# Kernel optimization log

Hardware: AMD Instinct MI355X
Metric: run time of the kernel (lower is better)

## Reference

```python
import jax, jax.numpy as jnp
import numpy as np

H = 5  # LSTM hidden size


def _lstm_layer(x, Wih, Whh, bih, bhh):
    # x: [B, T, D]; Wih: [4H, D]; Whh: [4H, H]; biases: [4H]
    B, T, _ = x.shape
    # precompute input contribution with one big GEMM (torch gate order i,f,g,o)
    xg = jnp.einsum('btd,gd->btg', x, Wih) + bih + bhh  # [B,T,4H]
    xg = jnp.swapaxes(xg, 0, 1)  # [T,B,4H]
    WhhT = Whh.T

    def step(carry, g_t):
        h, c = carry
        g = g_t + h @ WhhT
        i, f, gg, o = jnp.split(g, 4, axis=-1)
        i = jax.nn.sigmoid(i)
        f = jax.nn.sigmoid(f)
        gg = jnp.tanh(gg)
        o = jax.nn.sigmoid(o)
        c = f * c + i * gg
        h = o * jnp.tanh(c)
        return (h, c), h

    h0 = jnp.zeros((B, H), x.dtype)
    c0 = jnp.zeros((B, H), x.dtype)
    _, hs = jax.lax.scan(step, (h0, c0), xg)
    return jnp.swapaxes(hs, 0, 1)  # [B,T,H]


def _stacked_lstm(x, params):
    for (Wih, Whh, bih, bhh) in params:
        x = _lstm_layer(x, Wih, Whh, bih, bhh)
    return x


def setup_inputs() -> dict:
    key = jax.random.key(0)
    ks = jax.random.split(key, 24)
    B, T, D = 512, 1024, 225
    s = 1.0 / np.sqrt(H)

    def u(k, shape):
        return jax.random.uniform(k, shape, jnp.float32, -s, s)

    inp = {"x": jax.random.normal(ks[0], (B, T, D), jnp.float32)}
    # lstm1: layer0 input D=225, layer1 input H=5
    inp["l1_Wih0"] = u(ks[1], (4 * H, D)); inp["l1_Whh0"] = u(ks[2], (4 * H, H))
    inp["l1_bih0"] = u(ks[3], (4 * H,)); inp["l1_bhh0"] = u(ks[4], (4 * H,))
    inp["l1_Wih1"] = u(ks[5], (4 * H, H)); inp["l1_Whh1"] = u(ks[6], (4 * H, H))
    inp["l1_bih1"] = u(ks[7], (4 * H,)); inp["l1_bhh1"] = u(ks[8], (4 * H,))
    inp["fc1_W"] = u(ks[9], (H, H)); inp["fc1_b"] = u(ks[10], (H,))
    # lstm2: both layers input H=5
    inp["l2_Wih0"] = u(ks[11], (4 * H, H)); inp["l2_Whh0"] = u(ks[12], (4 * H, H))
    inp["l2_bih0"] = u(ks[13], (4 * H,)); inp["l2_bhh0"] = u(ks[14], (4 * H,))
    inp["l2_Wih1"] = u(ks[15], (4 * H, H)); inp["l2_Whh1"] = u(ks[16], (4 * H, H))
    inp["l2_bih1"] = u(ks[17], (4 * H,)); inp["l2_bhh1"] = u(ks[18], (4 * H,))
    inp["fc2_W"] = u(ks[19], (H, H)); inp["fc2_b"] = u(ks[20], (H,))
    return inp


def reference(x, l1_Wih0, l1_Whh0, l1_bih0, l1_bhh0,
              l1_Wih1, l1_Whh1, l1_bih1, l1_bhh1,
              fc1_W, fc1_b,
              l2_Wih0, l2_Whh0, l2_bih0, l2_bhh0,
              l2_Wih1, l2_Whh1, l2_bih1, l2_bhh1,
              fc2_W, fc2_b):
    # dropout layers are identity in inference mode
    h = _stacked_lstm(x, [(l1_Wih0, l1_Whh0, l1_bih0, l1_bhh0),
                          (l1_Wih1, l1_Whh1, l1_bih1, l1_bhh1)])
    h = jax.nn.relu(h @ fc1_W.T + fc1_b)
    h = _stacked_lstm(h, [(l2_Wih0, l2_Whh0, l2_bih0, l2_bhh0),
                          (l2_Wih1, l2_Whh1, l2_bih1, l2_bhh1)])
    return jax.nn.sigmoid(h @ fc2_W.T + fc2_b)
```

## Files before the change

kernel.cpp:

```cpp
#include <hip/hip_runtime.h>
#include <math.h>

#define T_STEPS 1024
#define B_SIZE  512
#define D_IN    225
#define WT_K    228
#define LOG2E   1.4426950408889634f

typedef float f32x2 __attribute__((ext_vector_type(2)));

__device__ __forceinline__ float fexp2(float x) {
#if __has_builtin(__builtin_amdgcn_exp2f)
  return __builtin_amdgcn_exp2f(x);
#else
  return exp2f(x);
#endif
}
__device__ __forceinline__ float frcp(float x) {
#if __has_builtin(__builtin_amdgcn_rcpf)
  return __builtin_amdgcn_rcpf(x);
#else
  return 1.0f / x;
#endif
}
#define SIG(x) frcp(1.0f + fexp2((x) * (-LOG2E)))
#define TH(x)  fmaf(2.0f, frcp(1.0f + fexp2((x) * (-2.0f * LOG2E))), -1.0f)

#define GL16(gp, lp) __builtin_amdgcn_global_load_lds(                          \
    (const __attribute__((address_space(1))) void*)(gp),                        \
    (__attribute__((address_space(3))) void*)(lp), 16, 0, 0)
#define GL4(gp, lp)  __builtin_amdgcn_global_load_lds(                          \
    (const __attribute__((address_space(1))) void*)(gp),                        \
    (__attribute__((address_space(3))) void*)(lp), 4, 0, 0)

#define WAIT_VM0() do {                                                         \
    asm volatile("s_waitcnt vmcnt(0)" ::: "memory");                            \
    __builtin_amdgcn_sched_barrier(0);                                          \
  } while (0)
#define WAIT_VM10() do {                                                        \
    asm volatile("s_waitcnt vmcnt(10)" ::: "memory");                           \
    __builtin_amdgcn_sched_barrier(0);                                          \
  } while (0)

__global__ __launch_bounds__(256)
void prep_wt(const float* __restrict__ Wih, const float* __restrict__ bih,
             const float* __restrict__ bhh, float* __restrict__ wt2)
{
  int i = blockIdx.x * 256 + threadIdx.x;
  int g = i / WT_K, kk = i - g * WT_K;
  float v = 0.f;
  if (g < 20 && kk < 225) v = Wih[g * 225 + kk];
  if (i >= 4560 && i < 4580) v = bih[i - 4560] + bhh[i - 4560];
  wt2[i] = v;
}

__global__ __launch_bounds__(256)
void xg_gemm(const float* __restrict__ x, const float* __restrict__ wtg,
             float* __restrict__ xg)
{
  __shared__ __align__(16) float xs[64 * D_IN];
  __shared__ __align__(16) float wt[4608];
  const int tid  = threadIdx.x;
  const int lane = tid & 63;
  const int w    = __builtin_amdgcn_readfirstlane(tid >> 6);

  {
    int n0 = (w < 2) ? 5 : 4;
    int c0 = (w < 2) ? w * 5 : 10 + (w - 2) * 4;
    for (int m = 0; m < n0; ++m)
      GL16(wtg + (c0 + m) * 256 + lane * 4, wt + (c0 + m) * 256);
  }
  {
    const float* src = x + (size_t)blockIdx.x * (64 * D_IN);
    for (int m = 0; m < 14; ++m)
      GL16(src + (w * 14 + m) * 256 + lane * 4, xs + (w * 14 + m) * 256);
    if (w == 0) GL4(src + 14336 + lane, xs + 14336);
  }
  __syncthreads();

  const float* wr = wt + (5 * w) * WT_K;
  float acc[5];
#pragma unroll
  for (int j = 0; j < 5; ++j) acc[j] = wt[4560 + 5 * w + j];
  const float* xr = xs + lane * D_IN;

#pragma unroll 8
  for (int kb = 0; kb < 224; kb += 4) {
    float x0 = xr[kb], x1 = xr[kb + 1], x2 = xr[kb + 2], x3 = xr[kb + 3];
#pragma unroll
    for (int j = 0; j < 5; ++j) {
      const float4 wv = *(const float4*)(wr + j * WT_K + kb);
      acc[j] = fmaf(x0, wv.x, acc[j]);
      acc[j] = fmaf(x1, wv.y, acc[j]);
      acc[j] = fmaf(x2, wv.z, acc[j]);
      acc[j] = fmaf(x3, wv.w, acc[j]);
    }
  }
  {
    float xl = xr[224];
#pragma unroll
    for (int j = 0; j < 5; ++j) acc[j] = fmaf(xl, wr[j * WT_K + 224], acc[j]);
  }
  float* op = xg + ((size_t)blockIdx.x * 64 + lane) * 20 + w;
#pragma unroll
  for (int j = 0; j < 5; ++j) op[4 * j] = acc[j];
}

__global__ __launch_bounds__(64)
void lstm_fused(const float* __restrict__ xg, float* __restrict__ out,
              const float* __restrict__ l1_Whh0,
              const float* __restrict__ l1_Wih1, const float* __restrict__ l1_Whh1,
              const float* __restrict__ l1_bih1, const float* __restrict__ l1_bhh1,
              const float* __restrict__ fc1_W,  const float* __restrict__ fc1_b,
              const float* __restrict__ l2_Wih0, const float* __restrict__ l2_Whh0,
              const float* __restrict__ l2_bih0, const float* __restrict__ l2_bhh0,
              const float* __restrict__ l2_Wih1, const float* __restrict__ l2_Whh1,
              const float* __restrict__ l2_bih1, const float* __restrict__ l2_bhh1,
              const float* __restrict__ fc2_W,  const float* __restrict__ fc2_b)
{
  __shared__ __align__(16) float xq[2][2][1280];
  __shared__ float outb[2][64][5];
  const int lane  = threadIdx.x & 63;
  const int half  = lane >> 5;
  const int l32   = lane & 31;
  const int stage = (l32 < 30) ? (l32 / 5) : 6;
  const int u     = (l32 < 30) ? (l32 - stage * 5) : 0;
  const int b0    = blockIdx.x * 2;

  const bool is_l0   = (stage == 0);
  const bool is_relu = (stage == 2);
  const bool is_fc   = (stage == 2) || (stage == 5);
  const bool is_fc2  = (stage == 5);

  float wi[4][5] = {}, wh[4][5] = {}, bs[4] = {};
  if (stage == 0) {
#pragma unroll
    for (int q = 0; q < 4; ++q)
#pragma unroll
      for (int j = 0; j < 5; ++j) wh[q][j] = l1_Whh0[(u + 5 * q) * 5 + j];
  } else if (stage == 1) {
#pragma unroll
    for (int q = 0; q < 4; ++q) {
#pragma unroll
      for (int j = 0; j < 5; ++j) {
        wi[q][j] = l1_Wih1[(u + 5 * q) * 5 + j];
        wh[q][j] = l1_Whh1[(u + 5 * q) * 5 + j];
      }
      bs[q] = l1_bih1[u + 5 * q] + l1_bhh1[u + 5 * q];
    }
  } else if (stage == 3) {
#pragma unroll
    for (int q = 0; q < 4; ++q) {
#pragma unroll
      for (int j = 0; j < 5; ++j) {
        wi[q][j] = l2_Wih0[(u + 5 * q) * 5 + j];
        wh[q][j] = l2_Whh0[(u + 5 * q) * 5 + j];
      }
      bs[q] = l2_bih0[u + 5 * q] + l2_bhh0[u + 5 * q];
    }
  } else if (stage == 4) {
#pragma unroll
    for (int q = 0; q < 4; ++q) {
#pragma unroll
      for (int j = 0; j < 5; ++j) {
        wi[q][j] = l2_Wih1[(u + 5 * q) * 5 + j];
        wh[q][j] = l2_Whh1[(u + 5 * q) * 5 + j];
      }
      bs[q] = l2_bih1[u + 5 * q] + l2_bhh1[u + 5 * q];
    }
  } else if (stage == 2) {
#pragma unroll
    for (int j = 0; j < 5; ++j) wi[0][j] = fc1_W[u * 5 + j];
    bs[0] = fc1_b[u];
  } else if (stage == 5) {
#pragma unroll
    for (int j = 0; j < 5; ++j) wi[0][j] = fc2_W[u * 5 + j];
    bs[0] = fc2_b[u];
  }

  f32x2 wi01[5], wi23[5], wh01[5], wh23[5];
#pragma unroll
  for (int j = 0; j < 5; ++j) {
    wi01[j] = f32x2{wi[0][j], wi[1][j]};
    wi23[j] = f32x2{wi[2][j], wi[3][j]};
    wh01[j] = f32x2{wh[0][j], wh[1][j]};
    wh23[j] = f32x2{wh[2][j], wh[3][j]};
  }
  const f32x2 bs01 = f32x2{bs[0], bs[1]};
  const f32x2 bs23 = f32x2{bs[2], bs[3]};

  int ii[5], ih[5];
  const int bse = half * 32;
  const int inb = (stage >= 1 && stage <= 5) ? (stage - 1) * 5 : 0;
  const int hb_ = (stage <= 5) ? stage * 5 : 0;
#pragma unroll
  for (int j = 0; j < 5; ++j) {
    ii[j] = (bse + inb + j) * 4;
    ih[j] = (bse + hb_ + j) * 4;
  }

  const float* obf = &outb[0][0][0];
  float* outbase = out + (size_t)b0 * T_STEPS * 5;
  int lof[10], ofs[10];
  bool fg1[10], fg2[10];
#pragma unroll
  for (int i2 = 0; i2 < 10; ++i2) {
    int idx = i2 * 64 + lane;
    int e  = (idx >= 320) ? 1 : 0;
    int r  = idx - e * 320;
    int tq = r / 5;
    int j2 = r - tq * 5;
    lof[i2] = e * 320 + (((tq - 5) & 63) * 5) + j2;
    ofs[i2] = e * (T_STEPS * 5) + tq * 5 + j2;
    fg1[i2] = (tq >= 5);
    fg2[i2] = (tq < 5);
  }

  const float* src0 = xg + (size_t)(b0 + 0) * T_STEPS * 20;
  const float* src1 = xg + (size_t)(b0 + 1) * T_STEPS * 20;

#define STAGE_CHUNK(CH, BUF)                                                   \
  { const float* s0_ = src0 + (CH) * 1280;                                     \
    const float* s1_ = src1 + (CH) * 1280;                                     \
    float* d0_ = &xq[BUF][0][0];                                               \
    float* d1_ = &xq[BUF][1][0];                                               \
    _Pragma("unroll")                                                          \
    for (int m = 0; m < 5; ++m) {                                              \
      GL16(s0_ + m * 256 + lane * 4, d0_ + m * 256);                           \
      GL16(s1_ + m * 256 + lane * 4, d1_ + m * 256);                           \
    } }

#define TICK(QV, GUARDED, KVAL)                                                \
  { const int hvi_ = __float_as_int(hv);                                       \
    float inx[5], hhx[5];                                                      \
    _Pragma("unroll")                                                          \
    for (int j = 0; j < 5; ++j) {                                              \
      inx[j] = __int_as_float(__builtin_amdgcn_ds_bpermute(ii[j], hvi_));      \
      hhx[j] = __int_as_float(__builtin_amdgcn_ds_bpermute(ih[j], hvi_));      \
    }                                                                          \
    f32x2 a01 = is_l0 ? f32x2{(QV).x, (QV).y} : bs01;                          \
    f32x2 a23 = is_l0 ? f32x2{(QV).z, (QV).w} : bs23;                          \
    f32x2 b01, b23;                                                            \
    { const f32x2 h0 = f32x2{hhx[0], hhx[0]};                                  \
      b01 = wh01[0] * h0; b23 = wh23[0] * h0; }                                \
    _Pragma("unroll")                                                          \
    for (int j = 0; j < 5; ++j) {                                              \
      const f32x2 xj = f32x2{inx[j], inx[j]};                                  \
      a01 = __builtin_elementwise_fma(wi01[j], xj, a01);                       \
      a23 = __builtin_elementwise_fma(wi23[j], xj, a23);                       \
    }                                                                          \
    _Pragma("unroll")                                                          \
    for (int j = 1; j < 5; ++j) {                                              \
      const f32x2 hj = f32x2{hhx[j], hhx[j]};                                  \
      b01 = __builtin_elementwise_fma(wh01[j], hj, b01);                       \
      b23 = __builtin_elementwise_fma(wh23[j], hj, b23);                       \
    }                                                                          \
    const f32x2 pre01 = a01 + b01, pre23 = a23 + b23;                          \
    float i_ = SIG(pre01.x), f_ = SIG(pre01.y);                                \
    float g_ = TH(pre23.x),  o_ = SIG(pre23.y);                                \
    float cn = fmaf(f_, c, i_ * g_);                                           \
    float hl = o_ * TH(cn);                                                    \
    float fx = is_relu ? fmaxf(pre01.x, 0.0f) : i_;                            \
    float hn = is_fc ? fx : hl;                                                \
    if (GUARDED) { bool ok = (KVAL) >= stage; c = ok ? cn : c; hv = ok ? hn : hv; } \
    else         { c = cn; hv = hn; }                                          \
    if (is_fc2) outb[half][((KVAL) + 59) & 63][u] = i_;                        \
  }

#define LQ(T) (*(const float4*)(xqb + 20 * (T)))
#define MINQ(X) (((X) > 63) ? 63 : (X))

#define CHUNK_BODY(GUARDED)                                                    \
  { float4 qA = LQ(0), qB = LQ(1), qC = LQ(2), qD = LQ(3);                     \
    _Pragma("unroll")                                                          \
    for (int g4 = 0; g4 < 16; ++g4) {                                          \
      const int kk = g4 * 4;                                                   \
      TICK(qA, GUARDED, kk + 0)                                                \
      qA = LQ(MINQ(kk + 4));                                                   \
      TICK(qB, GUARDED, kk + 1)                                                \
      qB = LQ(MINQ(kk + 5));                                                   \
      TICK(qC, GUARDED, kk + 2)                                                \
      qC = LQ(MINQ(kk + 6));                                                   \
      TICK(qD, GUARDED, kk + 3)                                                \
      qD = LQ(MINQ(kk + 7));                                                   \
    } }

#define FLUSH(TBASE, MODE)                                                     \
  { _Pragma("unroll")                                                          \
    for (int i2 = 0; i2 < 10; ++i2) {                                          \
      float v = obf[lof[i2]];                                                  \
      bool ok = (MODE == 0) || ((MODE == 1) ? fg1[i2] : fg2[i2]);              \
      if (ok) outbase[ofs[i2] + (TBASE) * 5] = v;                              \
    } }

  float hv = 0.f, c = 0.f;

  STAGE_CHUNK(0, 0)
  WAIT_VM0();

  {
    STAGE_CHUNK(1, 1)
    const float* xqb = &xq[0][half][4 * u];
    CHUNK_BODY(true)
    FLUSH(-5, 1)
    WAIT_VM10();
  }
  for (int ch = 1; ch < 16; ++ch) {
    if (ch < 15) STAGE_CHUNK(ch + 1, (ch + 1) & 1)
    const float* xqb = &xq[ch & 1][half][4 * u];
    CHUNK_BODY(false)
    FLUSH(ch * 64 - 5, 0)
    WAIT_VM10();
  }
  {
    const float* xqb = &xq[0][half][4 * u];
    float4 qZ = LQ(0);
    TICK(qZ, false, 0)
    TICK(qZ, false, 1)
    TICK(qZ, false, 2)
    TICK(qZ, false, 3)
    TICK(qZ, false, 4)
    FLUSH(T_STEPS - 5, 2)
  }

#undef STAGE_CHUNK
#undef TICK
#undef LQ
#undef MINQ
#undef CHUNK_BODY
#undef FLUSH
}

extern "C" void kernel_launch(void* const* d_in, const int* in_sizes, int n_in,
                              void* d_out, int out_size, void* d_ws, size_t ws_size,
                              hipStream_t stream)
{
  const float* x        = (const float*)d_in[0];
  const float* l1_Wih0  = (const float*)d_in[1];
  const float* l1_Whh0  = (const float*)d_in[2];
  const float* l1_bih0  = (const float*)d_in[3];
  const float* l1_bhh0  = (const float*)d_in[4];
  const float* l1_Wih1  = (const float*)d_in[5];
  const float* l1_Whh1  = (const float*)d_in[6];
  const float* l1_bih1  = (const float*)d_in[7];
  const float* l1_bhh1  = (const float*)d_in[8];
  const float* fc1_W    = (const float*)d_in[9];
  const float* fc1_b    = (const float*)d_in[10];
  const float* l2_Wih0  = (const float*)d_in[11];
  const float* l2_Whh0  = (const float*)d_in[12];
  const float* l2_bih0  = (const float*)d_in[13];
  const float* l2_bhh0  = (const float*)d_in[14];
  const float* l2_Wih1  = (const float*)d_in[15];
  const float* l2_Whh1  = (const float*)d_in[16];
  const float* l2_bih1  = (const float*)d_in[17];
  const float* l2_bhh1  = (const float*)d_in[18];
  const float* fc2_W    = (const float*)d_in[19];
  const float* fc2_b    = (const float*)d_in[20];

  float* xg   = (float*)d_ws;
  float* wtws = xg + 10485760;
  float* out  = (float*)d_out;

  prep_wt<<<dim3(18), dim3(256), 0, stream>>>(l1_Wih0, l1_bih0, l1_bhh0, wtws);

  xg_gemm<<<dim3((B_SIZE * T_STEPS) / 64), dim3(256), 0, stream>>>(x, wtws, xg);

  lstm_fused<<<dim3(B_SIZE / 2), dim3(64), 0, stream>>>(
      xg, out, l1_Whh0, l1_Wih1, l1_Whh1, l1_bih1, l1_bhh1,
      fc1_W, fc1_b, l2_Wih0, l2_Whh0, l2_bih0, l2_bhh0,
      l2_Wih1, l2_Whh1, l2_bih1, l2_bhh1, fc2_W, fc2_b);
}
```

Baseline: 419.3 us.

## Restructure input GEMM to one wave per block and simplify LSTM tick loop

The input-projection GEMM now runs one 64-lane wave per block. That wave computes all 20 gates with packed FMA against a k-major transposed weight layout and writes each row as float4. This replaces four waves that each handled five gates, cutting block-level sync and making the output stores contiguous. The LSTM recurrent loop drops the four-deep register prefetch of xg rows in favour of a pointer-advancing tick with a plain LDS load, and the output ring index is simplified. The trade-offs are less parallelism per block in the GEMM, more LDS traffic per thread, and a possible loss of latency hiding in the serial recurrence.

```diff
diff --git a/kernel.cpp b/kernel.cpp
--- a/kernel.cpp
+++ b/kernel.cpp
@@ -4,7 +4,6 @@
 #define T_STEPS 1024
 #define B_SIZE  512
 #define D_IN    225
-#define WT_K    228
 #define LOG2E   1.4426950408889634f
 
 typedef float f32x2 __attribute__((ext_vector_type(2)));
@@ -47,63 +46,73 @@
              const float* __restrict__ bhh, float* __restrict__ wt2)
 {
   int i = blockIdx.x * 256 + threadIdx.x;
-  int g = i / WT_K, kk = i - g * WT_K;
   float v = 0.f;
-  if (g < 20 && kk < 225) v = Wih[g * 225 + kk];
-  if (i >= 4560 && i < 4580) v = bih[i - 4560] + bhh[i - 4560];
+  if (i < 4500) {
+    int k = i / 20, g = i - k * 20;
+    v = Wih[g * D_IN + k];
+  } else if (i < 4520) {
+    v = bih[i - 4500] + bhh[i - 4500];
+  }
   wt2[i] = v;
 }
 
-__global__ __launch_bounds__(256)
+__global__ __launch_bounds__(64)
 void xg_gemm(const float* __restrict__ x, const float* __restrict__ wtg,
              float* __restrict__ xg)
 {
   __shared__ __align__(16) float xs[64 * D_IN];
   __shared__ __align__(16) float wt[4608];
-  const int tid  = threadIdx.x;
-  const int lane = tid & 63;
-  const int w    = __builtin_amdgcn_readfirstlane(tid >> 6);
-
-  {
-    int n0 = (w < 2) ? 5 : 4;
-    int c0 = (w < 2) ? w * 5 : 10 + (w - 2) * 4;
-    for (int m = 0; m < n0; ++m)
-      GL16(wtg + (c0 + m) * 256 + lane * 4, wt + (c0 + m) * 256);
-  }
+  const int lane = threadIdx.x;
+
+#pragma unroll
+  for (int m = 0; m < 18; ++m)
+    GL16(wtg + m * 256 + lane * 4, wt + m * 256);
   {
     const float* src = x + (size_t)blockIdx.x * (64 * D_IN);
-    for (int m = 0; m < 14; ++m)
-      GL16(src + (w * 14 + m) * 256 + lane * 4, xs + (w * 14 + m) * 256);
-    if (w == 0) GL4(src + 14336 + lane, xs + 14336);
-  }
-  __syncthreads();
-
-  const float* wr = wt + (5 * w) * WT_K;
-  float acc[5];
-#pragma unroll
-  for (int j = 0; j < 5; ++j) acc[j] = wt[4560 + 5 * w + j];
+#pragma unroll
+    for (int m = 0; m < 56; ++m)
+      GL16(src + m * 256 + lane * 4, xs + m * 256);
+    GL4(src + 14336 + lane, xs + 14336);
+  }
+  WAIT_VM0();
+
+  f32x2 acc2[10];
+#pragma unroll
+  for (int p = 0; p < 10; ++p)
+    acc2[p] = f32x2{wt[4500 + 2 * p], wt[4500 + 2 * p + 1]};
   const float* xr = xs + lane * D_IN;
 
-#pragma unroll 8
-  for (int kb = 0; kb < 224; kb += 4) {
-    float x0 = xr[kb], x1 = xr[kb + 1], x2 = xr[kb + 2], x3 = xr[kb + 3];
-#pragma unroll
-    for (int j = 0; j < 5; ++j) {
-      const float4 wv = *(const float4*)(wr + j * WT_K + kb);
-      acc[j] = fmaf(x0, wv.x, acc[j]);
-      acc[j] = fmaf(x1, wv.y, acc[j]);
-      acc[j] = fmaf(x2, wv.z, acc[j]);
-      acc[j] = fmaf(x3, wv.w, acc[j]);
-    }
-  }
-  {
-    float xl = xr[224];
-#pragma unroll
-    for (int j = 0; j < 5; ++j) acc[j] = fmaf(xl, wr[j * WT_K + 224], acc[j]);
-  }
-  float* op = xg + ((size_t)blockIdx.x * 64 + lane) * 20 + w;
-#pragma unroll
-  for (int j = 0; j < 5; ++j) op[4 * j] = acc[j];
+#pragma unroll 5
+  for (int k = 0; k < D_IN; ++k) {
+    const float xv = xr[k];
+    const f32x2 xv2 = f32x2{xv, xv};
+    const float* wk = wt + k * 20;
+    const float4 wA = *(const float4*)(wk);
+    const float4 wB = *(const float4*)(wk + 4);
+    const float4 wC = *(const float4*)(wk + 8);
+    const float4 wD = *(const float4*)(wk + 12);
+    const float4 wE = *(const float4*)(wk + 16);
+    acc2[0] = __builtin_elementwise_fma(f32x2{wA.x, wA.y}, xv2, acc2[0]);
+    acc2[1] = __builtin_elementwise_fma(f32x2{wA.z, wA.w}, xv2, acc2[1]);
+    acc2[2] = __builtin_elementwise_fma(f32x2{wB.x, wB.y}, xv2, acc2[2]);
+    acc2[3] = __builtin_elementwise_fma(f32x2{wB.z, wB.w}, xv2, acc2[3]);
+    acc2[4] = __builtin_elementwise_fma(f32x2{wC.x, wC.y}, xv2, acc2[4]);
+    acc2[5] = __builtin_elementwise_fma(f32x2{wC.z, wC.w}, xv2, acc2[5]);
+    acc2[6] = __builtin_elementwise_fma(f32x2{wD.x, wD.y}, xv2, acc2[6]);
+    acc2[7] = __builtin_elementwise_fma(f32x2{wD.z, wD.w}, xv2, acc2[7]);
+    acc2[8] = __builtin_elementwise_fma(f32x2{wE.x, wE.y}, xv2, acc2[8]);
+    acc2[9] = __builtin_elementwise_fma(f32x2{wE.z, wE.w}, xv2, acc2[9]);
+  }
+
+#define AG(G) (((G) & 1) ? acc2[(G) >> 1].y : acc2[(G) >> 1].x)
+  float* op = xg + ((size_t)blockIdx.x * 64 + lane) * 20;
+#pragma unroll
+  for (int q = 0; q < 5; ++q) {
+    float4 o;
+    o.x = AG(q); o.y = AG(5 + q); o.z = AG(10 + q); o.w = AG(15 + q);
+    *(float4*)(op + 4 * q) = o;
+  }
+#undef AG
 }
 
 __global__ __launch_bounds__(64)
@@ -210,7 +219,7 @@
     int r  = idx - e * 320;
     int tq = r / 5;
     int j2 = r - tq * 5;
-    lof[i2] = e * 320 + (((tq - 5) & 63) * 5) + j2;
+    lof[i2] = e * 320 + tq * 5 + j2;
     ofs[i2] = e * (T_STEPS * 5) + tq * 5 + j2;
     fg1[i2] = (tq >= 5);
     fg2[i2] = (tq < 5);
@@ -230,16 +239,17 @@
       GL16(s1_ + m * 256 + lane * 4, d1_ + m * 256);                           \
     } }
 
-#define TICK(QV, GUARDED, KVAL)                                                \
-  { const int hvi_ = __float_as_int(hv);                                       \
+#define TICKR(GUARDED, KK)                                                     \
+  { const float4 Qv = *(const float4*)xqp;                                     \
+    const int hvi_ = __float_as_int(hv);                                       \
     float inx[5], hhx[5];                                                      \
     _Pragma("unroll")                                                          \
     for (int j = 0; j < 5; ++j) {                                              \
       inx[j] = __int_as_float(__builtin_amdgcn_ds_bpermute(ii[j], hvi_));      \
       hhx[j] = __int_as_float(__builtin_amdgcn_ds_bpermute(ih[j], hvi_));      \
     }                                                                          \
-    f32x2 a01 = is_l0 ? f32x2{(QV).x, (QV).y} : bs01;                          \
-    f32x2 a23 = is_l0 ? f32x2{(QV).z, (QV).w} : bs23;                          \
+    f32x2 a01 = is_l0 ? f32x2{Qv.x, Qv.y} : bs01;                              \
+    f32x2 a23 = is_l0 ? f32x2{Qv.z, Qv.w} : bs23;                              \
     f32x2 b01, b23;                                                            \
     { const f32x2 h0 = f32x2{hhx[0], hhx[0]};                                  \
       b01 = wh01[0] * h0; b23 = wh23[0] * h0; }                                \
@@ -262,28 +272,10 @@
     float hl = o_ * TH(cn);                                                    \
     float fx = is_relu ? fmaxf(pre01.x, 0.0f) : i_;                            \
     float hn = is_fc ? fx : hl;                                                \
-    if (GUARDED) { bool ok = (KVAL) >= stage; c = ok ? cn : c; hv = ok ? hn : hv; } \
+    if (GUARDED) { bool ok = (KK) >= stage; c = ok ? cn : c; hv = ok ? hn : hv; } \
     else         { c = cn; hv = hn; }                                          \
-    if (is_fc2) outb[half][((KVAL) + 59) & 63][u] = i_;                        \
-  }
-
-#define LQ(T) (*(const float4*)(xqb + 20 * (T)))
-#define MINQ(X) (((X) > 63) ? 63 : (X))
-
-#define CHUNK_BODY(GUARDED)                                                    \
-  { float4 qA = LQ(0), qB = LQ(1), qC = LQ(2), qD = LQ(3);                     \
-    _Pragma("unroll")                                                          \
-    for (int g4 = 0; g4 < 16; ++g4) {                                          \
-      const int kk = g4 * 4;                                                   \
-      TICK(qA, GUARDED, kk + 0)                                                \
-      qA = LQ(MINQ(kk + 4));                                                   \
-      TICK(qB, GUARDED, kk + 1)                                                \
-      qB = LQ(MINQ(kk + 5));                                                   \
-      TICK(qC, GUARDED, kk + 2)                                                \
-      qC = LQ(MINQ(kk + 6));                                                   \
-      TICK(qD, GUARDED, kk + 3)                                                \
-      qD = LQ(MINQ(kk + 7));                                                   \
-    } }
+    if (is_fc2) outb[half][KK][u] = i_;                                        \
+    xqp += 20; }
 
 #define FLUSH(TBASE, MODE)                                                     \
   { _Pragma("unroll")                                                          \
@@ -294,40 +286,31 @@
     } }
 
   float hv = 0.f, c = 0.f;
+  const float* xqp;
 
   STAGE_CHUNK(0, 0)
   WAIT_VM0();
 
-  {
-    STAGE_CHUNK(1, 1)
-    const float* xqb = &xq[0][half][4 * u];
-    CHUNK_BODY(true)
-    FLUSH(-5, 1)
-    WAIT_VM10();
-  }
+  STAGE_CHUNK(1, 1)
+  xqp = &xq[0][half][4 * u];
+  for (int kk = 0; kk < 64; ++kk) TICKR(true, kk)
+  FLUSH(-5, 1)
+  WAIT_VM10();
+
   for (int ch = 1; ch < 16; ++ch) {
     if (ch < 15) STAGE_CHUNK(ch + 1, (ch + 1) & 1)
-    const float* xqb = &xq[ch & 1][half][4 * u];
-    CHUNK_BODY(false)
+    xqp = &xq[ch & 1][half][4 * u];
+#pragma unroll 2
+    for (int kk = 0; kk < 64; ++kk) TICKR(false, kk)
     FLUSH(ch * 64 - 5, 0)
     WAIT_VM10();
   }
-  {
-    const float* xqb = &xq[0][half][4 * u];
-    float4 qZ = LQ(0);
-    TICK(qZ, false, 0)
-    TICK(qZ, false, 1)
-    TICK(qZ, false, 2)
-    TICK(qZ, false, 3)
-    TICK(qZ, false, 4)
-    FLUSH(T_STEPS - 5, 2)
-  }
+  xqp = &xq[0][half][4 * u];
+  for (int kk = 0; kk < 5; ++kk) TICKR(false, kk)
+  FLUSH(T_STEPS - 5, 2)
 
 #undef STAGE_CHUNK
-#undef TICK
-#undef LQ
-#undef MINQ
-#undef CHUNK_BODY
+#undef TICKR
 #undef FLUSH
 }
 
@@ -363,7 +346,7 @@
 
   prep_wt<<<dim3(18), dim3(256), 0, stream>>>(l1_Wih0, l1_bih0, l1_bhh0, wtws);
 
-  xg_gemm<<<dim3((B_SIZE * T_STEPS) / 64), dim3(256), 0, stream>>>(x, wtws, xg);
+  xg_gemm<<<dim3((B_SIZE * T_STEPS) / 64), dim3(64), 0, stream>>>(x, wtws, xg);
 
   lstm_fused<<<dim3(B_SIZE / 2), dim3(64), 0, stream>>>(
       xg, out, l1_Whh0, l1_Wih1, l1_Whh1, l1_bih1, l1_bhh1,
```

After: 452.5 us. +7.9%, slower.

## Decouple layer-input shuffles from recurrence by adding a one-tick lag per stage

Applied to the files above, without the earlier changes.

Each tick now uses the inter-stage input value fetched in the previous tick, so stage s runs two steps behind stage s-1 instead of one. The input-side FMAs and the shuffles for the next tick leave the recurrent critical path, and only the hidden-state permutes and gate math remain serial. The pipeline fill and drain grow from 5 to 10 steps, the output lag and flush offsets change to match, and the hand-unrolled prefetch of the xg queue is replaced by a pointer-increment load with unroll 2.

```diff
diff --git a/kernel.cpp b/kernel.cpp
--- a/kernel.cpp
+++ b/kernel.cpp
@@ -126,6 +126,7 @@
   const int stage = (l32 < 30) ? (l32 / 5) : 6;
   const int u     = (l32 < 30) ? (l32 - stage * 5) : 0;
   const int b0    = blockIdx.x * 2;
+  const int stg2  = stage * 2;
 
   const bool is_l0   = (stage == 0);
   const bool is_relu = (stage == 2);
@@ -210,10 +211,10 @@
     int r  = idx - e * 320;
     int tq = r / 5;
     int j2 = r - tq * 5;
-    lof[i2] = e * 320 + (((tq - 5) & 63) * 5) + j2;
+    lof[i2] = e * 320 + tq * 5 + j2;
     ofs[i2] = e * (T_STEPS * 5) + tq * 5 + j2;
-    fg1[i2] = (tq >= 5);
-    fg2[i2] = (tq < 5);
+    fg1[i2] = (tq >= 10);
+    fg2[i2] = (tq < 10);
   }
 
   const float* src0 = xg + (size_t)(b0 + 0) * T_STEPS * 20;
@@ -230,25 +231,27 @@
       GL16(s1_ + m * 256 + lane * 4, d1_ + m * 256);                           \
     } }
 
-#define TICK(QV, GUARDED, KVAL)                                                \
-  { const int hvi_ = __float_as_int(hv);                                       \
-    float inx[5], hhx[5];                                                      \
+#define TICK2(GUARDED, KK, INU, IND)                                           \
+  { const float4 Qv = *(const float4*)xqp;                                     \
+    const int hvi_ = __float_as_int(hv);                                       \
+    float hhx[5];                                                              \
+    _Pragma("unroll")                                                          \
+    for (int j = 0; j < 5; ++j)                                                \
+      hhx[j] = __int_as_float(__builtin_amdgcn_ds_bpermute(ih[j], hvi_));      \
+    f32x2 a01 = is_l0 ? f32x2{Qv.x, Qv.y} : bs01;                              \
+    f32x2 a23 = is_l0 ? f32x2{Qv.z, Qv.w} : bs23;                              \
     _Pragma("unroll")                                                          \
     for (int j = 0; j < 5; ++j) {                                              \
-      inx[j] = __int_as_float(__builtin_amdgcn_ds_bpermute(ii[j], hvi_));      \
-      hhx[j] = __int_as_float(__builtin_amdgcn_ds_bpermute(ih[j], hvi_));      \
+      const f32x2 xj = f32x2{INU[j], INU[j]};                                  \
+      a01 = __builtin_elementwise_fma(wi01[j], xj, a01);                       \
+      a23 = __builtin_elementwise_fma(wi23[j], xj, a23);                       \
     }                                                                          \
-    f32x2 a01 = is_l0 ? f32x2{(QV).x, (QV).y} : bs01;                          \
-    f32x2 a23 = is_l0 ? f32x2{(QV).z, (QV).w} : bs23;                          \
+    _Pragma("unroll")                                                          \
+    for (int j = 0; j < 5; ++j)                                                \
+      IND[j] = __int_as_float(__builtin_amdgcn_ds_bpermute(ii[j], hvi_));      \
     f32x2 b01, b23;                                                            \
     { const f32x2 h0 = f32x2{hhx[0], hhx[0]};                                  \
       b01 = wh01[0] * h0; b23 = wh23[0] * h0; }                                \
-    _Pragma("unroll")                                                          \
-    for (int j = 0; j < 5; ++j) {                                              \
-      const f32x2 xj = f32x2{inx[j], inx[j]};                                  \
-      a01 = __builtin_elementwise_fma(wi01[j], xj, a01);                       \
-      a23 = __builtin_elementwise_fma(wi23[j], xj, a23);                       \
-    }                                                                          \
     _Pragma("unroll")                                                          \
     for (int j = 1; j < 5; ++j) {                                              \
       const f32x2 hj = f32x2{hhx[j], hhx[j]};                                  \
@@ -262,28 +265,10 @@
     float hl = o_ * TH(cn);                                                    \
     float fx = is_relu ? fmaxf(pre01.x, 0.0f) : i_;                            \
     float hn = is_fc ? fx : hl;                                                \
-    if (GUARDED) { bool ok = (KVAL) >= stage; c = ok ? cn : c; hv = ok ? hn : hv; } \
+    if (GUARDED) { bool ok = (KK) >= stg2; c = ok ? cn : c; hv = ok ? hn : hv; } \
     else         { c = cn; hv = hn; }                                          \
-    if (is_fc2) outb[half][((KVAL) + 59) & 63][u] = i_;                        \
-  }
-
-#define LQ(T) (*(const float4*)(xqb + 20 * (T)))
-#define MINQ(X) (((X) > 63) ? 63 : (X))
-
-#define CHUNK_BODY(GUARDED)                                                    \
-  { float4 qA = LQ(0), qB = LQ(1), qC = LQ(2), qD = LQ(3);                     \
-    _Pragma("unroll")                                                          \
-    for (int g4 = 0; g4 < 16; ++g4) {                                          \
-      const int kk = g4 * 4;                                                   \
-      TICK(qA, GUARDED, kk + 0)                                                \
-      qA = LQ(MINQ(kk + 4));                                                   \
-      TICK(qB, GUARDED, kk + 1)                                                \
-      qB = LQ(MINQ(kk + 5));                                                   \
-      TICK(qC, GUARDED, kk + 2)                                                \
-      qC = LQ(MINQ(kk + 6));                                                   \
-      TICK(qD, GUARDED, kk + 3)                                                \
-      qD = LQ(MINQ(kk + 7));                                                   \
-    } }
+    if (is_fc2) outb[half][KK][u] = i_;                                        \
+    xqp += 20; }
 
 #define FLUSH(TBASE, MODE)                                                     \
   { _Pragma("unroll")                                                          \
@@ -294,40 +279,43 @@
     } }
 
   float hv = 0.f, c = 0.f;
+  float inxA[5] = {0, 0, 0, 0, 0};
+  float inxB[5] = {0, 0, 0, 0, 0};
+  const float* xqp;
 
   STAGE_CHUNK(0, 0)
   WAIT_VM0();
 
-  {
-    STAGE_CHUNK(1, 1)
-    const float* xqb = &xq[0][half][4 * u];
-    CHUNK_BODY(true)
-    FLUSH(-5, 1)
-    WAIT_VM10();
-  }
+  STAGE_CHUNK(1, 1)
+  xqp = &xq[0][half][4 * u];
+#pragma unroll 2
+  for (int kk = 0; kk < 64; kk += 2) {
+    TICK2(true, kk,     inxA, inxB)
+    TICK2(true, kk + 1, inxB, inxA)
+  }
+  FLUSH(-10, 1)
+  WAIT_VM10();
+
   for (int ch = 1; ch < 16; ++ch) {
     if (ch < 15) STAGE_CHUNK(ch + 1, (ch + 1) & 1)
-    const float* xqb = &xq[ch & 1][half][4 * u];
-    CHUNK_BODY(false)
-    FLUSH(ch * 64 - 5, 0)
+    xqp = &xq[ch & 1][half][4 * u];
+#pragma unroll 2
+    for (int kk = 0; kk < 64; kk += 2) {
+      TICK2(false, kk,     inxA, inxB)
+      TICK2(false, kk + 1, inxB, inxA)
+    }
+    FLUSH(ch * 64 - 10, 0)
     WAIT_VM10();
   }
-  {
-    const float* xqb = &xq[0][half][4 * u];
-    float4 qZ = LQ(0);
-    TICK(qZ, false, 0)
-    TICK(qZ, false, 1)
-    TICK(qZ, false, 2)
-    TICK(qZ, false, 3)
-    TICK(qZ, false, 4)
-    FLUSH(T_STEPS - 5, 2)
-  }
+  xqp = &xq[0][half][4 * u];
+  for (int kk = 0; kk < 10; kk += 2) {
+    TICK2(false, kk,     inxA, inxB)
+    TICK2(false, kk + 1, inxB, inxA)
+  }
+  FLUSH(T_STEPS - 10, 2)
 
 #undef STAGE_CHUNK
-#undef TICK
-#undef LQ
-#undef MINQ
-#undef CHUNK_BODY
+#undef TICK2
 #undef FLUSH
 }
 
```

New measurement: 435.2 us. 1.04x slower.

## Fuse input-projection GEMM into LSTM kernel with producer waves

Applied to the files above, without the earlier changes.

Removes the separate xg_gemm kernel and its 40MB intermediate xg buffer. The LSTM kernel now launches 256 threads per block: wave 0 runs the recurrent chain while waves 1 and 2 each load a 64-step slab of x for one batch element into LDS. Those producer waves compute the 20 gate pre-activations with packed FMAs against a k-major weight layout and double-buffer the results into xq for the next chunk. This trades an extra global round trip for per-chunk __syncthreads, much larger LDS use (about 140KB), and a producer that may stall the serial recurrence if its GEMM is slower than a chunk of ticks.

```diff
diff --git a/kernel.cpp b/kernel.cpp
--- a/kernel.cpp
+++ b/kernel.cpp
@@ -4,7 +4,6 @@
 #define T_STEPS 1024
 #define B_SIZE  512
 #define D_IN    225
-#define WT_K    228
 #define LOG2E   1.4426950408889634f
 
 typedef float f32x2 __attribute__((ext_vector_type(2)));
@@ -37,77 +36,25 @@
     asm volatile("s_waitcnt vmcnt(0)" ::: "memory");                            \
     __builtin_amdgcn_sched_barrier(0);                                          \
   } while (0)
-#define WAIT_VM10() do {                                                        \
-    asm volatile("s_waitcnt vmcnt(10)" ::: "memory");                           \
-    __builtin_amdgcn_sched_barrier(0);                                          \
-  } while (0)
 
 __global__ __launch_bounds__(256)
 void prep_wt(const float* __restrict__ Wih, const float* __restrict__ bih,
              const float* __restrict__ bhh, float* __restrict__ wt2)
 {
   int i = blockIdx.x * 256 + threadIdx.x;
-  int g = i / WT_K, kk = i - g * WT_K;
   float v = 0.f;
-  if (g < 20 && kk < 225) v = Wih[g * 225 + kk];
-  if (i >= 4560 && i < 4580) v = bih[i - 4560] + bhh[i - 4560];
+  if (i < 4500) {
+    int k = i / 20, g = i - k * 20;
+    v = Wih[g * D_IN + k];
+  } else if (i < 4520) {
+    v = bih[i - 4500] + bhh[i - 4500];
+  }
   wt2[i] = v;
 }
 
 __global__ __launch_bounds__(256)
-void xg_gemm(const float* __restrict__ x, const float* __restrict__ wtg,
-             float* __restrict__ xg)
-{
-  __shared__ __align__(16) float xs[64 * D_IN];
-  __shared__ __align__(16) float wt[4608];
-  const int tid  = threadIdx.x;
-  const int lane = tid & 63;
-  const int w    = __builtin_amdgcn_readfirstlane(tid >> 6);
-
-  {
-    int n0 = (w < 2) ? 5 : 4;
-    int c0 = (w < 2) ? w * 5 : 10 + (w - 2) * 4;
-    for (int m = 0; m < n0; ++m)
-      GL16(wtg + (c0 + m) * 256 + lane * 4, wt + (c0 + m) * 256);
-  }
-  {
-    const float* src = x + (size_t)blockIdx.x * (64 * D_IN);
-    for (int m = 0; m < 14; ++m)
-      GL16(src + (w * 14 + m) * 256 + lane * 4, xs + (w * 14 + m) * 256);
-    if (w == 0) GL4(src + 14336 + lane, xs + 14336);
-  }
-  __syncthreads();
-
-  const float* wr = wt + (5 * w) * WT_K;
-  float acc[5];
-#pragma unroll
-  for (int j = 0; j < 5; ++j) acc[j] = wt[4560 + 5 * w + j];
-  const float* xr = xs + lane * D_IN;
-
-#pragma unroll 8
-  for (int kb = 0; kb < 224; kb += 4) {
-    float x0 = xr[kb], x1 = xr[kb + 1], x2 = xr[kb + 2], x3 = xr[kb + 3];
-#pragma unroll
-    for (int j = 0; j < 5; ++j) {
-      const float4 wv = *(const float4*)(wr + j * WT_K + kb);
-      acc[j] = fmaf(x0, wv.x, acc[j]);
-      acc[j] = fmaf(x1, wv.y, acc[j]);
-      acc[j] = fmaf(x2, wv.z, acc[j]);
-      acc[j] = fmaf(x3, wv.w, acc[j]);
-    }
-  }
-  {
-    float xl = xr[224];
-#pragma unroll
-    for (int j = 0; j < 5; ++j) acc[j] = fmaf(xl, wr[j * WT_K + 224], acc[j]);
-  }
-  float* op = xg + ((size_t)blockIdx.x * 64 + lane) * 20 + w;
-#pragma unroll
-  for (int j = 0; j < 5; ++j) op[4 * j] = acc[j];
-}
-
-__global__ __launch_bounds__(64)
-void lstm_fused(const float* __restrict__ xg, float* __restrict__ out,
+void lstm_fused(const float* __restrict__ x, const float* __restrict__ wtg,
+              float* __restrict__ out,
               const float* __restrict__ l1_Whh0,
               const float* __restrict__ l1_Wih1, const float* __restrict__ l1_Whh1,
               const float* __restrict__ l1_bih1, const float* __restrict__ l1_bhh1,
@@ -119,8 +66,12 @@
               const float* __restrict__ fc2_W,  const float* __restrict__ fc2_b)
 {
   __shared__ __align__(16) float xq[2][2][1280];
+  __shared__ __align__(16) float xsl[2][14400];
+  __shared__ __align__(16) float wt[4608];
   __shared__ float outb[2][64][5];
-  const int lane  = threadIdx.x & 63;
+  const int tid   = threadIdx.x;
+  const int lane  = tid & 63;
+  const int wv    = tid >> 6;
   const int half  = lane >> 5;
   const int l32   = lane & 31;
   const int stage = (l32 < 30) ? (l32 / 5) : 6;
@@ -216,18 +167,49 @@
     fg2[i2] = (tq < 5);
   }
 
-  const float* src0 = xg + (size_t)(b0 + 0) * T_STEPS * 20;
-  const float* src1 = xg + (size_t)(b0 + 1) * T_STEPS * 20;
-
-#define STAGE_CHUNK(CH, BUF)                                                   \
-  { const float* s0_ = src0 + (CH) * 1280;                                     \
-    const float* s1_ = src1 + (CH) * 1280;                                     \
-    float* d0_ = &xq[BUF][0][0];                                               \
-    float* d1_ = &xq[BUF][1][0];                                               \
-    _Pragma("unroll")                                                          \
-    for (int m = 0; m < 5; ++m) {                                              \
-      GL16(s0_ + m * 256 + lane * 4, d0_ + m * 256);                           \
-      GL16(s1_ + m * 256 + lane * 4, d1_ + m * 256);                           \
+#define AG(G) (((G) & 1) ? acc2[(G) >> 1].y : acc2[(G) >> 1].x)
+#define PRODUCE(CH, BUF)                                                       \
+  { const int e_ = wv - 1;                                                     \
+    const float* slab_ = x + ((size_t)(b0 + e_) * T_STEPS + (CH) * 64) * 225;  \
+    float* dst_ = &xsl[e_][0];                                                 \
+    _Pragma("unroll")                                                          \
+    for (int m_ = 0; m_ < 56; ++m_)                                            \
+      GL16(slab_ + m_ * 256 + lane * 4, dst_ + m_ * 256);                      \
+    GL4(slab_ + 14336 + lane, dst_ + 14336);                                   \
+    WAIT_VM0();                                                                \
+    f32x2 acc2[10];                                                            \
+    _Pragma("unroll")                                                          \
+    for (int p_ = 0; p_ < 10; ++p_)                                            \
+      acc2[p_] = f32x2{wt[4500 + 2 * p_], wt[4500 + 2 * p_ + 1]};              \
+    const float* xr_ = dst_ + lane * 225;                                      \
+    _Pragma("unroll 3")                                                        \
+    for (int k_ = 0; k_ < 225; ++k_) {                                         \
+      const float xv_ = xr_[k_];                                               \
+      const f32x2 xv2_ = f32x2{xv_, xv_};                                      \
+      const float* wk_ = wt + k_ * 20;                                         \
+      const float4 wA_ = *(const float4*)(wk_);                                \
+      const float4 wB_ = *(const float4*)(wk_ + 4);                            \
+      const float4 wC_ = *(const float4*)(wk_ + 8);                            \
+      const float4 wD_ = *(const float4*)(wk_ + 12);                           \
+      const float4 wE_ = *(const float4*)(wk_ + 16);                           \
+      acc2[0] = __builtin_elementwise_fma(f32x2{wA_.x, wA_.y}, xv2_, acc2[0]); \
+      acc2[1] = __builtin_elementwise_fma(f32x2{wA_.z, wA_.w}, xv2_, acc2[1]); \
+      acc2[2] = __builtin_elementwise_fma(f32x2{wB_.x, wB_.y}, xv2_, acc2[2]); \
+      acc2[3] = __builtin_elementwise_fma(f32x2{wB_.z, wB_.w}, xv2_, acc2[3]); \
+      acc2[4] = __builtin_elementwise_fma(f32x2{wC_.x, wC_.y}, xv2_, acc2[4]); \
+      acc2[5] = __builtin_elementwise_fma(f32x2{wC_.z, wC_.w}, xv2_, acc2[5]); \
+      acc2[6] = __builtin_elementwise_fma(f32x2{wD_.x, wD_.y}, xv2_, acc2[6]); \
+      acc2[7] = __builtin_elementwise_fma(f32x2{wD_.z, wD_.w}, xv2_, acc2[7]); \
+      acc2[8] = __builtin_elementwise_fma(f32x2{wE_.x, wE_.y}, xv2_, acc2[8]); \
+      acc2[9] = __builtin_elementwise_fma(f32x2{wE_.z, wE_.w}, xv2_, acc2[9]); \
+    }                                                                          \
+    float* qp_ = &xq[BUF][e_][lane * 20];                                      \
+    _Pragma("unroll")                                                          \
+    for (int u_ = 0; u_ < 5; ++u_) {                                           \
+      float4 o_;                                                               \
+      o_.x = AG(u_);      o_.y = AG(5 + u_);                                   \
+      o_.z = AG(10 + u_); o_.w = AG(15 + u_);                                  \
+      *(float4*)(qp_ + 4 * u_) = o_;                                           \
     } }
 
 #define TICK(QV, GUARDED, KVAL)                                                \
@@ -295,24 +277,31 @@
 
   float hv = 0.f, c = 0.f;
 
-  STAGE_CHUNK(0, 0)
-  WAIT_VM0();
-
-  {
-    STAGE_CHUNK(1, 1)
-    const float* xqb = &xq[0][half][4 * u];
-    CHUNK_BODY(true)
-    FLUSH(-5, 1)
-    WAIT_VM10();
-  }
-  for (int ch = 1; ch < 16; ++ch) {
-    if (ch < 15) STAGE_CHUNK(ch + 1, (ch + 1) & 1)
-    const float* xqb = &xq[ch & 1][half][4 * u];
-    CHUNK_BODY(false)
-    FLUSH(ch * 64 - 5, 0)
-    WAIT_VM10();
-  }
-  {
+  if (wv == 1 || wv == 2) {
+    for (int m = wv - 1; m < 18; m += 2)
+      GL16(wtg + m * 256 + lane * 4, wt + m * 256);
+    WAIT_VM0();
+  }
+  __syncthreads();
+  if (wv == 1 || wv == 2) PRODUCE(0, 0)
+  __syncthreads();
+
+  for (int ch = 0; ch < 16; ++ch) {
+    if (wv == 0) {
+      const float* xqb = &xq[ch & 1][half][4 * u];
+      if (ch == 0) {
+        CHUNK_BODY(true)
+        FLUSH(-5, 1)
+      } else {
+        CHUNK_BODY(false)
+        FLUSH(ch * 64 - 5, 0)
+      }
+    } else if ((wv == 1 || wv == 2) && ch < 15) {
+      PRODUCE(ch + 1, (ch + 1) & 1)
+    }
+    __syncthreads();
+  }
+  if (wv == 0) {
     const float* xqb = &xq[0][half][4 * u];
     float4 qZ = LQ(0);
     TICK(qZ, false, 0)
@@ -323,7 +312,8 @@
     FLUSH(T_STEPS - 5, 2)
   }
 
-#undef STAGE_CHUNK
+#undef AG
+#undef PRODUCE
 #undef TICK
 #undef LQ
 #undef MINQ
@@ -357,16 +347,13 @@
   const float* fc2_W    = (const float*)d_in[19];
   const float* fc2_b    = (const float*)d_in[20];
 
-  float* xg   = (float*)d_ws;
-  float* wtws = xg + 10485760;
+  float* wtws = (float*)d_ws;
   float* out  = (float*)d_out;
 
   prep_wt<<<dim3(18), dim3(256), 0, stream>>>(l1_Wih0, l1_bih0, l1_bhh0, wtws);
 
-  xg_gemm<<<dim3((B_SIZE * T_STEPS) / 64), dim3(256), 0, stream>>>(x, wtws, xg);
-
-  lstm_fused<<<dim3(B_SIZE / 2), dim3(64), 0, stream>>>(
-      xg, out, l1_Whh0, l1_Wih1, l1_Whh1, l1_bih1, l1_bhh1,
+  lstm_fused<<<dim3(B_SIZE / 2), dim3(256), 0, stream>>>(
+      x, wtws, out, l1_Whh0, l1_Wih1, l1_Whh1, l1_bih1, l1_bhh1,
       fc1_W, fc1_b, l2_Wih0, l2_Whh0, l2_bih0, l2_bhh0,
       l2_Wih1, l2_Whh1, l2_bih1, l2_bhh1, fc2_W, fc2_b);
 }
```

Result: faster. 350.5 us (-16.4%).
